# Kernel optimization log

Hardware: AMD Instinct MI355X
Metric: run time of the kernel (lower is better)

## Reference

```python
import jax, jax.numpy as jnp
import numpy as np

TEMPERATURE = 0.1  # init kwarg
EPS = 1e-8        # torch cosine_similarity eps


def setup_inputs() -> dict:
    key = jax.random.key(0)
    k1, k2, k3 = jax.random.split(key, 3)
    B, D, C = 4096, 1024, 32
    representations = jax.random.normal(k1, (B, D), dtype=jnp.float32)
    soft_labels = jax.random.uniform(k2, (B, C), dtype=jnp.float32)
    labels = jax.random.randint(k3, (B,), 0, 32, dtype=jnp.int64)
    return {
        "representations": representations,
        "soft_labels": soft_labels,
        "labels": labels,
        "pseudo_weight": 10,
    }


def reference(representations, soft_labels, labels, pseudo_weight):
    B = representations.shape[0]
    # row-normalize (cosine similarity)
    norms = jnp.maximum(jnp.linalg.norm(representations, axis=1, keepdims=True), EPS)
    rn = representations / norms
    Z = (rn @ rn.T) / TEMPERATURE                      # [B, B] scaled cosine sims
    E = jnp.exp(Z)
    off_diag = 1.0 - jnp.eye(B, dtype=Z.dtype)         # exclude j == i
    denom = jnp.sum(E * off_diag, axis=1, keepdims=True)   # [B, 1]
    loss_arr = -(Z - jnp.log(denom))                   # -log(exp(Z_ij)/denom_i)
    # positive-pair weights: same label, j != i (detached in original)
    pos = (labels[:, None] == labels[None, :]).astype(Z.dtype) * off_diag
    soft_sim = jax.lax.stop_gradient(soft_labels @ soft_labels.T)  # torch.inner, detached
    w = pos + pseudo_weight * soft_sim
    return jnp.sum(loss_arr * w) / B
```

## Files before the change

### kernel.cpp

```cpp
#include <hip/hip_runtime.h>
#include <hip/hip_bf16.h>
#include <stdint.h>


typedef float f32x4 __attribute__((ext_vector_type(4)));
typedef float f32x2 __attribute__((ext_vector_type(2)));
typedef long i64;

#define INV_T 10.0f
#define Z_SCALE (INV_T / 256.0f)

#define GLD16(gp, lp)                                                          \
    __builtin_amdgcn_global_load_lds(                                          \
        (const __attribute__((address_space(1))) uint32_t*)(gp),               \
        (__attribute__((address_space(3))) uint32_t*)(lp), 16, 0, 0)

#define OFF_RNF8  0
#define OFF_DENOM 4194304
#define OFF_POSS  (OFF_DENOM + 16384)
#define OFF_G     (OFF_POSS + 16384)
#define OFF_OACC  (OFF_G + 131072)
#define OFF_DONE  (OFF_OACC + 16)
#define ZERO_SPAN 167936
#define OFF_CSP   (OFF_DENOM + ZERO_SPAN)
#define OFF_CCP   (OFF_CSP + 4096)

__global__ __launch_bounds__(256) void scl_stage1(const float* __restrict__ rep,
                                                  const float* __restrict__ sl,
                                                  const int* __restrict__ labels,
                                                  uint32_t* __restrict__ rnf8,
                                                  float* __restrict__ cs_part,
                                                  int* __restrict__ cc_part,
                                                  char* __restrict__ zbase) {
    int b = blockIdx.x;
    int t = threadIdx.x;
    if (b < 4096) {
        int row = b;
        const float4* src = reinterpret_cast<const float4*>(rep + (size_t)row * 1024);
        float4 v = src[t];
        float s = v.x * v.x + v.y * v.y + v.z * v.z + v.w * v.w;
#pragma unroll
        for (int m = 1; m < 64; m <<= 1) s += __shfl_xor(s, m, 64);
        __shared__ float red[4];
        if ((t & 63) == 0) red[t >> 6] = s;
        __syncthreads();
        s = red[0] + red[1] + red[2] + red[3];
        float nf = 16.0f / fmaxf(sqrtf(s), 1e-8f);
        int p = 0;
        p = __builtin_amdgcn_cvt_pk_fp8_f32(v.x * nf, v.y * nf, p, false);
        p = __builtin_amdgcn_cvt_pk_fp8_f32(v.z * nf, v.w * nf, p, true);
        rnf8[row * 256 + t] = (uint32_t)p;
    } else if (b < 4128) {
        __shared__ float part[8][32];
        __shared__ int bins[32];
        int bb = b - 4096;
        if (t < 32) bins[t] = 0;
        __syncthreads();
        if (t < 128) atomicAdd(&bins[labels[bb * 128 + t]], 1);
        int c = t & 31, rg = t >> 5;
        float s = 0.f;
#pragma unroll 4
        for (int k = 0; k < 16; ++k) {
            int i = bb * 128 + rg * 16 + k;
            s += sl[i * 32 + c];
        }
        part[rg][c] = s;
        __syncthreads();
        if (t < 32) {
            float tot = 0.f;
#pragma unroll
            for (int g = 0; g < 8; ++g) tot += part[g][t];
            cs_part[bb * 32 + t] = tot;
            cc_part[bb * 32 + t] = bins[t];
        }
    } else {
        int zb = b - 4128;
        *(uint4*)(zbase + (size_t)zb * 4096 + t * 16) = (uint4){0, 0, 0, 0};
    }
}

__global__ __launch_bounds__(64) void scl_main(const uint8_t* __restrict__ rnf8,
                                               const float* __restrict__ sl,
                                               const int* __restrict__ labels,
                                               float* __restrict__ denom,
                                               float* __restrict__ posS,
                                               float* __restrict__ G) {
    int lane = threadIdx.x;

    if (blockIdx.x >= 2080) {
        int u = blockIdx.x - 2080;
        int dblk = u & 31, ks = u >> 5;
        int c = lane & 31, dq = lane >> 5;
        int d0 = dblk * 32 + dq * 16;
        f32x2 acc2[8];
#pragma unroll
        for (int j = 0; j < 8; ++j) acc2[j] = (f32x2){0.f, 0.f};
        int i0 = ks * 128;
#pragma unroll 2
        for (int k = 0; k < 128; ++k) {
            int i = i0 + k;
            uint4 rv = *(const uint4*)&rnf8[(size_t)i * 1024 + d0];
            float sv = sl[i * 32 + c];
            f32x2 sv2 = {sv, sv};
            acc2[0] += __builtin_amdgcn_cvt_pk_f32_fp8((int)rv.x, false) * sv2;
            acc2[1] += __builtin_amdgcn_cvt_pk_f32_fp8((int)rv.x, true) * sv2;
            acc2[2] += __builtin_amdgcn_cvt_pk_f32_fp8((int)rv.y, false) * sv2;
            acc2[3] += __builtin_amdgcn_cvt_pk_f32_fp8((int)rv.y, true) * sv2;
            acc2[4] += __builtin_amdgcn_cvt_pk_f32_fp8((int)rv.z, false) * sv2;
            acc2[5] += __builtin_amdgcn_cvt_pk_f32_fp8((int)rv.z, true) * sv2;
            acc2[6] += __builtin_amdgcn_cvt_pk_f32_fp8((int)rv.w, false) * sv2;
            acc2[7] += __builtin_amdgcn_cvt_pk_f32_fp8((int)rv.w, true) * sv2;
        }
#pragma unroll
        for (int j = 0; j < 8; ++j) {
            atomicAdd(&G[(d0 + 2 * j) * 32 + c], acc2[j][0] * 0.0625f);
            atomicAdd(&G[(d0 + 2 * j + 1) * 32 + c], acc2[j][1] * 0.0625f);
        }
        return;
    }

    __shared__ __align__(16) uint8_t Ls[16384];

    int L = blockIdx.x;
    int bi = 0, rem = L;
    while (rem >= 64 - bi) { rem -= 64 - bi; ++bi; }
    int bj = bi + rem;
    int rowA0 = bi * 64, colB0 = bj * 64;

    int m_ = lane & 15, g = lane >> 4;
    int r4 = lane >> 2;
    int csw = (lane & 3) ^ ((lane >> 3) & 3);
    const uint8_t* gA = rnf8 + (size_t)(rowA0 + r4) * 1024 + csw * 16;
    const uint8_t* gB = rnf8 + (size_t)(colB0 + r4) * 1024 + csw * 16;
    uint8_t* As = Ls;
    uint8_t* Bs = Ls + 4096;

#define ISSUE8(KT, NB)                                                         \
    {                                                                          \
        const uint8_t* pa = gA + (KT) * 64;                                    \
        const uint8_t* pb = gB + (KT) * 64;                                    \
        GLD16(pa,          As + (NB));                                         \
        GLD16(pa + 16384,  As + (NB) + 1024);                                  \
        GLD16(pa + 32768,  As + (NB) + 2048);                                  \
        GLD16(pa + 49152,  As + (NB) + 3072);                                  \
        GLD16(pb,          Bs + (NB));                                         \
        GLD16(pb + 16384,  Bs + (NB) + 1024);                                  \
        GLD16(pb + 32768,  Bs + (NB) + 2048);                                  \
        GLD16(pb + 49152,  Bs + (NB) + 3072);                                  \
    }

    f32x4 acc[4][4];
#pragma unroll
    for (int a = 0; a < 4; ++a)
#pragma unroll
        for (int b = 0; b < 4; ++b) acc[a][b] = (f32x4){0.f, 0.f, 0.f, 0.f};

    int fsw = (g ^ ((m_ >> 1) & 3)) * 16;

    ISSUE8(0, 0);
#pragma unroll
    for (int kt = 0; kt < 16; ++kt) {
        int cb = (kt & 1) * 8192;
        if (kt < 15) {
            ISSUE8(kt + 1, 8192 - cb);
            asm volatile("s_waitcnt vmcnt(8)" ::: "memory");
        } else {
            asm volatile("s_waitcnt vmcnt(0)" ::: "memory");
        }
        f32x4 aq[4], bq[4];
#pragma unroll
        for (int ti = 0; ti < 4; ++ti)
            aq[ti] = *(const f32x4*)&As[cb + (ti * 16 + m_) * 64 + fsw];
#pragma unroll
        for (int tj = 0; tj < 4; ++tj)
            bq[tj] = *(const f32x4*)&Bs[cb + (tj * 16 + m_) * 64 + fsw];
#pragma unroll
        for (int s = 0; s < 2; ++s)
#pragma unroll
            for (int ti = 0; ti < 4; ++ti)
#pragma unroll
                for (int tj = 0; tj < 4; ++tj) {
                    i64 a = ((const i64*)&aq[ti])[s];
                    i64 b = ((const i64*)&bq[tj])[s];
                    acc[ti][tj] = __builtin_amdgcn_mfma_f32_16x16x32_fp8_fp8(
                        a, b, acc[ti][tj], 0, 0, 0);
                }
    }
#undef ISSUE8

    bool isDiag = (bi == bj);
    int cl = m_;
    float colE[4] = {0.f, 0.f, 0.f, 0.f}, colP[4] = {0.f, 0.f, 0.f, 0.f};
    int lcj[4];
#pragma unroll
    for (int tj = 0; tj < 4; ++tj) lcj[tj] = labels[colB0 + tj * 16 + cl];
#pragma unroll
    for (int ti = 0; ti < 4; ++ti) {
        int rowLoc = ti * 16 + g * 4;
        float rE[4] = {0.f, 0.f, 0.f, 0.f}, rP[4] = {0.f, 0.f, 0.f, 0.f};
        int lr[4];
#pragma unroll
        for (int r = 0; r < 4; ++r) lr[r] = labels[rowA0 + rowLoc + r];
#pragma unroll
        for (int tj = 0; tj < 4; ++tj) {
            int gCol = colB0 + tj * 16 + cl;
            int lc = lcj[tj];
            f32x4 a = acc[ti][tj];
#pragma unroll
            for (int r = 0; r < 4; ++r) {
                int gRow = rowA0 + rowLoc + r;
                float z = Z_SCALE * a[r];
                float e = __expf(z);
                bool offd = (gRow != gCol);
                if (!offd) e = 0.f;
                rE[r] += e;
                colE[tj] += e;
                if (offd && (lr[r] == lc)) { rP[r] += z; colP[tj] += z; }
            }
        }
#pragma unroll
        for (int r = 0; r < 4; ++r) {
            float v = rE[r], p = rP[r];
#pragma unroll
            for (int msk = 1; msk < 16; msk <<= 1) {
                v += __shfl_xor(v, msk, 64);
                p += __shfl_xor(p, msk, 64);
            }
            if (cl == 0) {
                int gRow = rowA0 + rowLoc + r;
                atomicAdd(&denom[gRow], v);
                atomicAdd(&posS[gRow], p);
            }
        }
    }
    if (!isDiag) {
#pragma unroll
        for (int tj = 0; tj < 4; ++tj) {
            float v = colE[tj], p = colP[tj];
            v += __shfl_xor(v, 16, 64); p += __shfl_xor(p, 16, 64);
            v += __shfl_xor(v, 32, 64); p += __shfl_xor(p, 32, 64);
            if (g == 0) {
                int gCol = colB0 + tj * 16 + cl;
                atomicAdd(&denom[gCol], v);
                atomicAdd(&posS[gCol], p);
            }
        }
    }
}

__global__ __launch_bounds__(256) void scl_finalize(const float* __restrict__ denom,
                                                    const float* __restrict__ posS,
                                                    const float* __restrict__ sl,
                                                    const int* __restrict__ labels,
                                                    const float* __restrict__ cs_part,
                                                    const int* __restrict__ cc_part,
                                                    const float* __restrict__ G,
                                                    const int* __restrict__ pwp,
                                                    double* __restrict__ oacc,
                                                    int* __restrict__ done,
                                                    float* __restrict__ out) {
    int t = threadIdx.x;
    int bits = *pwp;
    float pw = (bits >= -(1 << 22) && bits <= (1 << 22)) ? (float)bits
                                                         : __int_as_float(bits);
    __shared__ double wsum[4];
    double contrib = 0.0;

    if (blockIdx.x < 8) {
        __shared__ __align__(16) float css[32];
        __shared__ int ccs[32];
        if (t < 32) {
            float s = 0.f; int n = 0;
#pragma unroll
            for (int b = 0; b < 32; ++b) {
                s += cs_part[b * 32 + t];
                n += cc_part[b * 32 + t];
            }
            css[t] = s; ccs[t] = n;
        }
        __syncthreads();
        const f32x4* sl4 = (const f32x4*)sl;
        const f32x4* cs4 = (const f32x4*)css;
        double td = 0.0;
#pragma unroll
        for (int h = 0; h < 2; ++h) {
            int i = blockIdx.x * 512 + h * 256 + t;
            float dW = 0.f;
#pragma unroll
            for (int q = 0; q < 8; ++q) {
                f32x4 s = sl4[i * 8 + q];
                f32x4 c = cs4[q];
                dW += s[0] * c[0] + s[1] * c[1] + s[2] * c[2] + s[3] * c[3];
            }
            float Wv = (float)(ccs[labels[i]] - 1) + pw * dW;
            td += (double)(__logf(denom[i]) * Wv - posS[i]);
        }
#pragma unroll
        for (int m = 1; m < 64; m <<= 1) td += __shfl_xor(td, m, 64);
        if ((t & 63) == 0) wsum[t >> 6] = td;
        __syncthreads();
        contrib = wsum[0] + wsum[1] + wsum[2] + wsum[3];
    } else {
        const f32x4* G4 = (const f32x4*)G;
        float gs = 0.f;
#pragma unroll
        for (int q = 0; q < 32; ++q) {
            f32x4 v = G4[q * 256 + t];
            gs += v[0] * v[0] + v[1] * v[1] + v[2] * v[2] + v[3] * v[3];
        }
        double gd = (double)gs;
#pragma unroll
        for (int m = 1; m < 64; m <<= 1) gd += __shfl_xor(gd, m, 64);
        if ((t & 63) == 0) wsum[t >> 6] = gd;
        __syncthreads();
        contrib = -(double)(pw * INV_T) * (wsum[0] + wsum[1] + wsum[2] + wsum[3]);
    }

    if (t == 0) {
        atomicAdd(oacc, contrib);
        __threadfence();
        int old = atomicAdd(done, 1);
        if (old == 8) {
            double tot = atomicAdd(oacc, 0.0);
            out[0] = (float)(tot * (1.0 / 4096.0));
        }
    }
}

extern "C" void kernel_launch(void* const* d_in, const int* in_sizes, int n_in,
                              void* d_out, int out_size, void* d_ws, size_t ws_size,
                              hipStream_t stream) {
    const float* rep = (const float*)d_in[0];
    const float* sl = (const float*)d_in[1];
    const int* labels = (const int*)d_in[2];
    const int* pwp = (const int*)d_in[3];

    char* ws = (char*)d_ws;
    uint8_t* rnf8 = (uint8_t*)(ws + OFF_RNF8);
    float* denom = (float*)(ws + OFF_DENOM);
    float* posS = (float*)(ws + OFF_POSS);
    float* G = (float*)(ws + OFF_G);
    double* oacc = (double*)(ws + OFF_OACC);
    int* done = (int*)(ws + OFF_DONE);
    float* cs_part = (float*)(ws + OFF_CSP);
    int* cc_part = (int*)(ws + OFF_CCP);

    scl_stage1<<<4169, 256, 0, stream>>>(rep, sl, labels, (uint32_t*)rnf8,
                                         cs_part, cc_part, ws + OFF_DENOM);
    scl_main<<<3104, 64, 0, stream>>>(rnf8, sl, labels, denom, posS, G);
    scl_finalize<<<9, 256, 0, stream>>>(denom, posS, sl, labels, cs_part, cc_part,
                                        G, pwp, oacc, done, (float*)d_out);
}
```

Baseline: 125.3 us.

## Pre-pack FP8 rows into MFMA fragment layout and load fragments directly to registers

Stage1 now normalizes 16 rows per block and writes the FP8 representation in a packed layout that matches the 16x16x32 MFMA operand fragments, so the Gram kernel loads each 8-byte fragment straight into registers with a register double-buffer instead of staging tiles through LDS with global_load_lds. The G-accumulation path is adapted to read the packed layout. This removes LDS traffic, LDS barriers and swizzle math from the main loop. The cost is more, smaller global loads per MFMA, no LDS reuse, and a reduction of stage1 parallelism from 4096 to 256 normalization blocks.

```diff
diff --git a/kernel.cpp b/kernel.cpp
--- a/kernel.cpp
+++ b/kernel.cpp
@@ -9,11 +9,6 @@
 
 #define INV_T 10.0f
 #define Z_SCALE (INV_T / 256.0f)
-
-#define GLD16(gp, lp)                                                          \
-    __builtin_amdgcn_global_load_lds(                                          \
-        (const __attribute__((address_space(1))) uint32_t*)(gp),               \
-        (__attribute__((address_space(3))) uint32_t*)(lp), 16, 0, 0)
 
 #define OFF_RNF8  0
 #define OFF_DENOM 4194304
@@ -28,32 +23,46 @@
 __global__ __launch_bounds__(256) void scl_stage1(const float* __restrict__ rep,
                                                   const float* __restrict__ sl,
                                                   const int* __restrict__ labels,
-                                                  uint32_t* __restrict__ rnf8,
+                                                  uint8_t* __restrict__ rnP,
                                                   float* __restrict__ cs_part,
                                                   int* __restrict__ cc_part,
                                                   char* __restrict__ zbase) {
     int b = blockIdx.x;
     int t = threadIdx.x;
-    if (b < 4096) {
-        int row = b;
-        const float4* src = reinterpret_cast<const float4*>(rep + (size_t)row * 1024);
-        float4 v = src[t];
-        float s = v.x * v.x + v.y * v.y + v.z * v.z + v.w * v.w;
-#pragma unroll
-        for (int m = 1; m < 64; m <<= 1) s += __shfl_xor(s, m, 64);
-        __shared__ float red[4];
-        if ((t & 63) == 0) red[t >> 6] = s;
-        __syncthreads();
-        s = red[0] + red[1] + red[2] + red[3];
+    if (b < 256) {
+        __shared__ uint32_t Ls32[4096];
+        int rl = t >> 4, i = t & 15;
+        int row = b * 16 + rl;
+        const float4* src = (const float4*)(rep + (size_t)row * 1024);
+        float s = 0.f;
+#pragma unroll
+        for (int j = 0; j < 16; ++j) {
+            float4 v = src[i + j * 16];
+            s += v.x * v.x + v.y * v.y + v.z * v.z + v.w * v.w;
+        }
+#pragma unroll
+        for (int m = 1; m < 16; m <<= 1) s += __shfl_xor(s, m, 64);
         float nf = 16.0f / fmaxf(sqrtf(s), 1e-8f);
-        int p = 0;
-        p = __builtin_amdgcn_cvt_pk_fp8_f32(v.x * nf, v.y * nf, p, false);
-        p = __builtin_amdgcn_cvt_pk_fp8_f32(v.z * nf, v.w * nf, p, true);
-        rnf8[row * 256 + t] = (uint32_t)p;
-    } else if (b < 4128) {
+        int g2 = (i >> 1) & 3;
+        int dw = ((g2 * 16 + rl) * 8 + (i & 1) * 4) >> 2;
+#pragma unroll
+        for (int j = 0; j < 16; ++j) {
+            float4 v = src[i + j * 16];
+            int pk = 0;
+            pk = __builtin_amdgcn_cvt_pk_fp8_f32(v.x * nf, v.y * nf, pk, false);
+            pk = __builtin_amdgcn_cvt_pk_fp8_f32(v.z * nf, v.w * nf, pk, true);
+            int kt = j * 2 + (i >> 3);
+            Ls32[kt * 128 + dw] = (uint32_t)pk;
+        }
+        __syncthreads();
+        uint4* dst = (uint4*)(rnP + (size_t)b * 16384);
+        const uint4* srcl = (const uint4*)Ls32;
+#pragma unroll
+        for (int q = 0; q < 4; ++q) dst[t * 4 + q] = srcl[t * 4 + q];
+    } else if (b < 288) {
         __shared__ float part[8][32];
         __shared__ int bins[32];
-        int bb = b - 4096;
+        int bb = b - 256;
         if (t < 32) bins[t] = 0;
         __syncthreads();
         if (t < 128) atomicAdd(&bins[labels[bb * 128 + t]], 1);
@@ -74,12 +83,12 @@
             cc_part[bb * 32 + t] = bins[t];
         }
     } else {
-        int zb = b - 4128;
+        int zb = b - 288;
         *(uint4*)(zbase + (size_t)zb * 4096 + t * 16) = (uint4){0, 0, 0, 0};
     }
 }
 
-__global__ __launch_bounds__(64) void scl_main(const uint8_t* __restrict__ rnf8,
+__global__ __launch_bounds__(64) void scl_main(const uint8_t* __restrict__ rnP,
                                                const float* __restrict__ sl,
                                                const int* __restrict__ labels,
                                                float* __restrict__ denom,
@@ -91,7 +100,6 @@
         int u = blockIdx.x - 2080;
         int dblk = u & 31, ks = u >> 5;
         int c = lane & 31, dq = lane >> 5;
-        int d0 = dblk * 32 + dq * 16;
         f32x2 acc2[8];
 #pragma unroll
         for (int j = 0; j < 8; ++j) acc2[j] = (f32x2){0.f, 0.f};
@@ -99,18 +107,22 @@
 #pragma unroll 2
         for (int k = 0; k < 128; ++k) {
             int i = i0 + k;
-            uint4 rv = *(const uint4*)&rnf8[(size_t)i * 1024 + d0];
+            const uint8_t* fb = rnP + (size_t)(i >> 4) * 16384 + dblk * 512 +
+                                (dq * 32 + (i & 15)) * 8;
+            uint2 r01 = *(const uint2*)fb;
+            uint2 r23 = *(const uint2*)(fb + 128);
             float sv = sl[i * 32 + c];
             f32x2 sv2 = {sv, sv};
-            acc2[0] += __builtin_amdgcn_cvt_pk_f32_fp8((int)rv.x, false) * sv2;
-            acc2[1] += __builtin_amdgcn_cvt_pk_f32_fp8((int)rv.x, true) * sv2;
-            acc2[2] += __builtin_amdgcn_cvt_pk_f32_fp8((int)rv.y, false) * sv2;
-            acc2[3] += __builtin_amdgcn_cvt_pk_f32_fp8((int)rv.y, true) * sv2;
-            acc2[4] += __builtin_amdgcn_cvt_pk_f32_fp8((int)rv.z, false) * sv2;
-            acc2[5] += __builtin_amdgcn_cvt_pk_f32_fp8((int)rv.z, true) * sv2;
-            acc2[6] += __builtin_amdgcn_cvt_pk_f32_fp8((int)rv.w, false) * sv2;
-            acc2[7] += __builtin_amdgcn_cvt_pk_f32_fp8((int)rv.w, true) * sv2;
-        }
+            acc2[0] += __builtin_amdgcn_cvt_pk_f32_fp8((int)r01.x, false) * sv2;
+            acc2[1] += __builtin_amdgcn_cvt_pk_f32_fp8((int)r01.x, true) * sv2;
+            acc2[2] += __builtin_amdgcn_cvt_pk_f32_fp8((int)r01.y, false) * sv2;
+            acc2[3] += __builtin_amdgcn_cvt_pk_f32_fp8((int)r01.y, true) * sv2;
+            acc2[4] += __builtin_amdgcn_cvt_pk_f32_fp8((int)r23.x, false) * sv2;
+            acc2[5] += __builtin_amdgcn_cvt_pk_f32_fp8((int)r23.x, true) * sv2;
+            acc2[6] += __builtin_amdgcn_cvt_pk_f32_fp8((int)r23.y, false) * sv2;
+            acc2[7] += __builtin_amdgcn_cvt_pk_f32_fp8((int)r23.y, true) * sv2;
+        }
+        int d0 = dblk * 32 + dq * 16;
 #pragma unroll
         for (int j = 0; j < 8; ++j) {
             atomicAdd(&G[(d0 + 2 * j) * 32 + c], acc2[j][0] * 0.0625f);
@@ -118,8 +130,6 @@
         }
         return;
     }
-
-    __shared__ __align__(16) uint8_t Ls[16384];
 
     int L = blockIdx.x;
     int bi = 0, rem = L;
@@ -128,65 +138,48 @@
     int rowA0 = bi * 64, colB0 = bj * 64;
 
     int m_ = lane & 15, g = lane >> 4;
-    int r4 = lane >> 2;
-    int csw = (lane & 3) ^ ((lane >> 3) & 3);
-    const uint8_t* gA = rnf8 + (size_t)(rowA0 + r4) * 1024 + csw * 16;
-    const uint8_t* gB = rnf8 + (size_t)(colB0 + r4) * 1024 + csw * 16;
-    uint8_t* As = Ls;
-    uint8_t* Bs = Ls + 4096;
-
-#define ISSUE8(KT, NB)                                                         \
+
+    const uint8_t* pa[4];
+    const uint8_t* pb[4];
+#pragma unroll
+    for (int ti = 0; ti < 4; ++ti) {
+        pa[ti] = rnP + (size_t)((rowA0 >> 4) + ti) * 16384 + lane * 8;
+        pb[ti] = rnP + (size_t)((colB0 >> 4) + ti) * 16384 + lane * 8;
+    }
+
+    f32x4 acc[4][4];
+#pragma unroll
+    for (int a = 0; a < 4; ++a)
+#pragma unroll
+        for (int b = 0; b < 4; ++b) acc[a][b] = (f32x4){0.f, 0.f, 0.f, 0.f};
+
+#define LOADK(KT, AA, BB)                                                      \
     {                                                                          \
-        const uint8_t* pa = gA + (KT) * 64;                                    \
-        const uint8_t* pb = gB + (KT) * 64;                                    \
-        GLD16(pa,          As + (NB));                                         \
-        GLD16(pa + 16384,  As + (NB) + 1024);                                  \
-        GLD16(pa + 32768,  As + (NB) + 2048);                                  \
-        GLD16(pa + 49152,  As + (NB) + 3072);                                  \
-        GLD16(pb,          Bs + (NB));                                         \
-        GLD16(pb + 16384,  Bs + (NB) + 1024);                                  \
-        GLD16(pb + 32768,  Bs + (NB) + 2048);                                  \
-        GLD16(pb + 49152,  Bs + (NB) + 3072);                                  \
-    }
-
-    f32x4 acc[4][4];
-#pragma unroll
-    for (int a = 0; a < 4; ++a)
-#pragma unroll
-        for (int b = 0; b < 4; ++b) acc[a][b] = (f32x4){0.f, 0.f, 0.f, 0.f};
-
-    int fsw = (g ^ ((m_ >> 1) & 3)) * 16;
-
-    ISSUE8(0, 0);
-#pragma unroll
-    for (int kt = 0; kt < 16; ++kt) {
-        int cb = (kt & 1) * 8192;
-        if (kt < 15) {
-            ISSUE8(kt + 1, 8192 - cb);
-            asm volatile("s_waitcnt vmcnt(8)" ::: "memory");
-        } else {
-            asm volatile("s_waitcnt vmcnt(0)" ::: "memory");
-        }
-        f32x4 aq[4], bq[4];
-#pragma unroll
-        for (int ti = 0; ti < 4; ++ti)
-            aq[ti] = *(const f32x4*)&As[cb + (ti * 16 + m_) * 64 + fsw];
-#pragma unroll
-        for (int tj = 0; tj < 4; ++tj)
-            bq[tj] = *(const f32x4*)&Bs[cb + (tj * 16 + m_) * 64 + fsw];
-#pragma unroll
-        for (int s = 0; s < 2; ++s)
-#pragma unroll
-            for (int ti = 0; ti < 4; ++ti)
-#pragma unroll
-                for (int tj = 0; tj < 4; ++tj) {
-                    i64 a = ((const i64*)&aq[ti])[s];
-                    i64 b = ((const i64*)&bq[tj])[s];
-                    acc[ti][tj] = __builtin_amdgcn_mfma_f32_16x16x32_fp8_fp8(
-                        a, b, acc[ti][tj], 0, 0, 0);
-                }
-    }
-#undef ISSUE8
+        _Pragma("unroll") for (int ti = 0; ti < 4; ++ti) {                     \
+            AA[ti] = *(const i64*)(pa[ti] + (KT) * 512);                       \
+            BB[ti] = *(const i64*)(pb[ti] + (KT) * 512);                       \
+        }                                                                      \
+    }
+#define MFMAB(AA, BB)                                                          \
+    {                                                                          \
+        _Pragma("unroll") for (int ti = 0; ti < 4; ++ti)                       \
+            _Pragma("unroll") for (int tj = 0; tj < 4; ++tj)                   \
+                acc[ti][tj] = __builtin_amdgcn_mfma_f32_16x16x32_fp8_fp8(      \
+                    AA[ti], BB[tj], acc[ti][tj], 0, 0, 0);                     \
+    }
+
+    i64 a0[4], b0[4], a1[4], b1[4];
+    LOADK(0, a0, b0);
+    LOADK(1, a1, b1);
+#pragma unroll
+    for (int kt = 0; kt < 32; kt += 2) {
+        MFMAB(a0, b0);
+        if (kt + 2 < 32) LOADK(kt + 2, a0, b0);
+        MFMAB(a1, b1);
+        if (kt + 3 < 32) LOADK(kt + 3, a1, b1);
+    }
+#undef LOADK
+#undef MFMAB
 
     bool isDiag = (bi == bj);
     int cl = m_;
@@ -336,7 +329,7 @@
     const int* pwp = (const int*)d_in[3];
 
     char* ws = (char*)d_ws;
-    uint8_t* rnf8 = (uint8_t*)(ws + OFF_RNF8);
+    uint8_t* rnP = (uint8_t*)(ws + OFF_RNF8);
     float* denom = (float*)(ws + OFF_DENOM);
     float* posS = (float*)(ws + OFF_POSS);
     float* G = (float*)(ws + OFF_G);
@@ -345,9 +338,9 @@
     float* cs_part = (float*)(ws + OFF_CSP);
     int* cc_part = (int*)(ws + OFF_CCP);
 
-    scl_stage1<<<4169, 256, 0, stream>>>(rep, sl, labels, (uint32_t*)rnf8,
-                                         cs_part, cc_part, ws + OFF_DENOM);
-    scl_main<<<3104, 64, 0, stream>>>(rnf8, sl, labels, denom, posS, G);
+    scl_stage1<<<329, 256, 0, stream>>>(rep, sl, labels, rnP, cs_part, cc_part,
+                                        ws + OFF_DENOM);
+    scl_main<<<3104, 64, 0, stream>>>(rnP, sl, labels, denom, posS, G);
     scl_finalize<<<9, 256, 0, stream>>>(denom, posS, sl, labels, cs_part, cc_part,
                                         G, pwp, oacc, done, (float*)d_out);
 }
```

New measurement: 130.8 us. +4.4%, slower.
